# Performance work log

Hardware: AMD Instinct MI355X
Metric: run time of the kernel (lower is better)

Reference implementation:

```python
import jax, jax.numpy as jnp
import numpy as np

B, S, D, H, E, K, DH = 4, 2048, 1024, 8, 8, 2, 128
ROPE_BASE = 10000.0


def setup_inputs() -> dict:
    key = jax.random.key(0)
    ks = jax.random.split(key, 7)
    s = 1.0 / np.sqrt(D)
    x = jax.random.normal(ks[0], (B, S, D), dtype=jnp.float32)
    Wq = jax.random.normal(ks[1], (H * DH, D), dtype=jnp.float32) * s
    Wk = jax.random.normal(ks[2], (H * DH, D), dtype=jnp.float32) * s
    Wv = jax.random.normal(ks[3], (H * E, D, DH), dtype=jnp.float32) * s
    Wo = jax.random.normal(ks[4], (H * E, DH, D), dtype=jnp.float32) * (1.0 / np.sqrt(H * DH))
    sel_v = jax.random.normal(ks[5], (H * E, D), dtype=jnp.float32) * s
    sel_o = jax.random.normal(ks[6], (H * E, D), dtype=jnp.float32) * s
    positions = jnp.broadcast_to(jnp.arange(S, dtype=jnp.int32), (B, S))
    return {"x": x, "Wq": Wq, "Wk": Wk, "Wv": Wv, "Wo": Wo,
            "sel_v": sel_v, "sel_o": sel_o, "positions": positions}


def _rope(t, pos, inv_freq):
    # t: [b,h,s,d], pos: [b,s]
    freqs = pos.astype(t.dtype)[:, :, None] * inv_freq          # [b,s,d/2]
    emb = jnp.concatenate([freqs, freqs], axis=-1)[:, None]      # [b,1,s,d]
    sin, cos = jnp.sin(emb), jnp.cos(emb)
    x1, x2 = jnp.split(t, 2, axis=-1)
    rot = jnp.concatenate([-x2, x1], axis=-1)
    return t * cos + rot * sin


def reference(x, Wq, Wk, Wv, Wo, sel_v, sel_o, positions):
    # dense shared Q/K projections -> [b,h,s,dh]
    q = (x @ Wq.T).reshape(B, S, H, DH).transpose(0, 2, 1, 3)
    k = (x @ Wk.T).reshape(B, S, H, DH).transpose(0, 2, 1, 3)

    # V expert routing (sigmoid, non-competitive top-k per head)
    gv = jax.nn.sigmoid((x @ sel_v.T).reshape(B, S, H, E))       # [b,s,h,e]
    vw, vi = jax.lax.top_k(gv, K)                                # [b,s,h,k]
    vall = jnp.einsum('bsm,hemd->bshed', x, Wv.reshape(H, E, D, DH))
    vsel = jnp.take_along_axis(vall, vi[..., None], axis=3)      # [b,s,h,k,dh]
    v = (vw[..., None] * vsel).sum(axis=3).transpose(0, 2, 1, 3)  # [b,h,s,dh]

    # RoPE (rotate_fraction=1 -> full head dim)
    inv_freq = 1.0 / (ROPE_BASE ** (jnp.arange(0, DH, 2, dtype=jnp.float32) / DH))
    q = _rope(q, positions, inv_freq)
    k = _rope(k, positions, inv_freq)

    # masked SDPA (causal bool mask, scale 1/sqrt(dh))
    scores = jnp.einsum('bhqd,bhkd->bhqk', q, k) * (1.0 / np.sqrt(DH))
    causal = jnp.tril(jnp.ones((S, S), dtype=bool))
    scores = jnp.where(causal, scores, jnp.finfo(scores.dtype).min)
    attn = jax.nn.softmax(scores, axis=-1)
    ctx = jnp.einsum('bhqk,bhkd->bqhd', attn, v)                  # [b,s,h,dh]

    # O expert routing, combine via scattered gate weights
    go = jax.nn.sigmoid((x @ sel_o.T).reshape(B, S, H, E))
    ow, oi = jax.lax.top_k(go, K)
    g_full = (ow[..., None] * jax.nn.one_hot(oi, E, dtype=x.dtype)).sum(axis=3)  # [b,s,h,e]
    out = jnp.einsum('bshd,bshe,hedm->bsm', ctx, g_full, Wo.reshape(H, E, DH, D))
    return out
```

## Files before the change

### kernel.cpp

```cpp
#include <hip/hip_runtime.h>
#include <math.h>

typedef unsigned short u16;
typedef unsigned int u32;
typedef __attribute__((ext_vector_type(8))) short short8;
typedef __attribute__((ext_vector_type(4))) float f32x4;

constexpr int cB = 4, cS = 2048, cD = 1024, cH = 8, cE = 8, cK = 2, cDH = 128;
constexpr int cBS = cB * cS;
constexpr int cHE = cH * cE;

__device__ inline u16 f2bf(float f) {
    u32 u = __float_as_uint(f);
    u += 0x7fffu + ((u >> 16) & 1u);
    return (u16)(u >> 16);
}
__device__ inline float bf2f(u16 h) { return __uint_as_float(((u32)h) << 16); }

__device__ inline void gload_lds16(const u16* g, u16* l) {
    __builtin_amdgcn_global_load_lds(
        (const __attribute__((address_space(1))) void*)g,
        (__attribute__((address_space(3))) void*)l, 16, 0, 0);
}

#define SWZ_RD(row, ks, quad) ((((quad) + ((ks) >> 3)) ^ ((row) & 7)) << 3)

__global__ __launch_bounds__(256) void k_cast_split(
    const float* __restrict__ src, u16* __restrict__ hi, u16* __restrict__ lo)
{
    const size_t i = (size_t)blockIdx.x * 256 + threadIdx.x;
    float4 v = ((const float4*)src)[i];
    u16 hx = f2bf(v.x), hy = f2bf(v.y), hz = f2bf(v.z), hw = f2bf(v.w);
    u16 lx = f2bf(v.x - bf2f(hx)), ly = f2bf(v.y - bf2f(hy));
    u16 lz = f2bf(v.z - bf2f(hz)), lw = f2bf(v.w - bf2f(hw));
    uint2 oh; oh.x = (u32)hx | ((u32)hy << 16); oh.y = (u32)hz | ((u32)hw << 16);
    uint2 ol; ol.x = (u32)lx | ((u32)ly << 16); ol.y = (u32)lz | ((u32)lw << 16);
    ((uint2*)hi)[i] = oh;
    ((uint2*)lo)[i] = ol;
}

__global__ __launch_bounds__(256, 2) void k_gemm_logits3(
    const u16* __restrict__ xh, const u16* __restrict__ xlo,
    const u16* __restrict__ selh, const u16* __restrict__ sell,
    float* __restrict__ lgp)
{
    __shared__ u16 As[128 * 64];
    __shared__ u16 Bs[128 * 64];
    const int r0 = blockIdx.x * 128;
    const int term = blockIdx.y;
    const u16* A = (term == 1) ? xlo : xh;
    const u16* B = (term == 2) ? sell : selh;
    float* outp = lgp + (size_t)term * cBS * 128;
    const int t = threadIdx.x;
    const int w = t >> 6, lane = t & 63;
    const int wm = w >> 1, wn = w & 1;
    const int quad = lane >> 4, lm = lane & 15;
    const int lr = lane >> 3;
    const int lcs = (((lane & 7) ^ lr) * 8);

    f32x4 acc[4][4];
#pragma unroll
    for (int i = 0; i < 4; i++)
#pragma unroll
        for (int j = 0; j < 4; j++)
#pragma unroll
            for (int r = 0; r < 4; r++) acc[i][j][r] = 0.0f;

    for (int kc = 0; kc < cD; kc += 64) {
#pragma unroll
        for (int p = 0; p < 4; p++) {
            const int rA = p * 32 + w * 8;
            gload_lds16(A + (size_t)(r0 + rA + lr) * cD + kc + lcs, As + rA * 64);
            gload_lds16(B + (size_t)(rA + lr) * cD + kc + lcs, Bs + rA * 64);
        }
        __syncthreads();
#pragma unroll
        for (int ks = 0; ks < 64; ks += 32) {
            short8 av[4], bv[4];
#pragma unroll
            for (int i = 0; i < 4; i++) {
                const int row = wm * 64 + i * 16 + lm;
                av[i] = *(const short8*)(As + row * 64 + SWZ_RD(row, ks, quad));
            }
#pragma unroll
            for (int j = 0; j < 4; j++) {
                const int row = wn * 64 + j * 16 + lm;
                bv[j] = *(const short8*)(Bs + row * 64 + SWZ_RD(row, ks, quad));
            }
#pragma unroll
            for (int i = 0; i < 4; i++)
#pragma unroll
                for (int j = 0; j < 4; j++)
                    acc[i][j] = __builtin_amdgcn_mfma_f32_16x16x32_bf16(av[i], bv[j], acc[i][j], 0, 0, 0);
        }
        __syncthreads();
    }
#pragma unroll
    for (int i = 0; i < 4; i++)
#pragma unroll
        for (int r = 0; r < 4; r++) {
            const int row = r0 + wm * 64 + i * 16 + quad * 4 + r;
#pragma unroll
            for (int j = 0; j < 4; j++)
                outp[(size_t)row * 128 + wn * 64 + j * 16 + lm] = acc[i][j][r];
        }
}

__global__ __launch_bounds__(256) void k_top2_flag(
    const float* __restrict__ lgp, float* __restrict__ gv_d, float* __restrict__ go_d,
    int* __restrict__ flags, int* __restrict__ counter)
{
    const int idx = blockIdx.x * 256 + threadIdx.x;
    const int row = idx >> 4, r16 = idx & 15;
    const int which = r16 >> 3, h = r16 & 7;
    const float* l0 = lgp + (size_t)row * 128 + which * 64 + h * 8;
    const float* l1 = l0 + (size_t)cBS * 128;
    const float* l2 = l1 + (size_t)cBS * 128;
    float v[8];
#pragma unroll
    for (int e = 0; e < cE; e++) v[e] = l0[e] + l1[e] + l2[e];
    int i0 = 0; float b0 = v[0];
#pragma unroll
    for (int e = 1; e < cE; e++) { if (v[e] > b0) { b0 = v[e]; i0 = e; } }
    int i1 = -1; float b1 = -3.0e38f;
#pragma unroll
    for (int e = 0; e < cE; e++) { if (e != i0 && v[e] > b1) { b1 = v[e]; i1 = e; } }
    float b2 = -3.0e38f;
#pragma unroll
    for (int e = 0; e < cE; e++) { if (e != i0 && e != i1 && v[e] > b2) b2 = v[e]; }
    const float w0 = 1.0f / (1.0f + __expf(-b0));
    const float w1 = 1.0f / (1.0f + __expf(-b1));
    float* dst = (which ? go_d : gv_d) + (size_t)row * 64 + h * 8;
#pragma unroll
    for (int e = 0; e < cE; e++)
        dst[e] = (e == i0) ? w0 : ((e == i1) ? w1 : 0.0f);
    if (b1 - b2 < 1.0e-3f) {
        const int s = atomicAdd(counter, 1);
        flags[s] = (row << 4) | r16;
    }
}

__global__ __launch_bounds__(64) void k_repair(
    const float* __restrict__ x, const float* __restrict__ sel_v,
    const float* __restrict__ sel_o,
    const int* __restrict__ counter, const int* __restrict__ flags,
    float* __restrict__ gv_d, float* __restrict__ go_d)
{
    const int n = *counter;
    const int lane = threadIdx.x;
    for (int it = blockIdx.x; it < n; it += gridDim.x) {
        const int item = flags[it];
        const int row = item >> 4, which = (item >> 3) & 1, h = item & 7;
        const float* xr = x + (size_t)row * cD;
        const float* sb = (which ? sel_o : sel_v) + (size_t)(h * 8) * cD;
        float lg[8];
#pragma unroll
        for (int e = 0; e < cE; e++) {
            float a = 0.0f;
#pragma unroll
            for (int dg = 0; dg < 4; dg++) {
                const int d = dg * 256 + lane * 4;
                const float4 xv = *(const float4*)(xr + d);
                const float4 sv = *(const float4*)(sb + (size_t)e * cD + d);
                a += xv.x * sv.x + xv.y * sv.y + xv.z * sv.z + xv.w * sv.w;
            }
#pragma unroll
            for (int off = 1; off < 64; off <<= 1) a += __shfl_xor(a, off);
            lg[e] = a;
        }
        int i0 = 0; float b0 = lg[0];
#pragma unroll
        for (int e = 1; e < cE; e++) { if (lg[e] > b0) { b0 = lg[e]; i0 = e; } }
        int i1 = -1; float b1 = -3.0e38f;
#pragma unroll
        for (int e = 0; e < cE; e++) { if (e != i0 && lg[e] > b1) { b1 = lg[e]; i1 = e; } }
        if (lane == 0) {
            const float w0 = 1.0f / (1.0f + expf(-b0));
            const float w1 = 1.0f / (1.0f + expf(-b1));
            float* dst = (which ? go_d : gv_d) + (size_t)row * 64 + h * 8;
#pragma unroll
            for (int e = 0; e < cE; e++)
                dst[e] = (e == i0) ? w0 : ((e == i1) ? w1 : 0.0f);
        }
    }
}

__global__ __launch_bounds__(256) void k_cast_f2b(
    const float* __restrict__ src, u16* __restrict__ dst)
{
    const size_t i = (size_t)blockIdx.x * 256 + threadIdx.x;
    float4 v = ((const float4*)src)[i];
    u32 lo = (u32)f2bf(v.x) | ((u32)f2bf(v.y) << 16);
    u32 hi = (u32)f2bf(v.z) | ((u32)f2bf(v.w) << 16);
    uint2 o; o.x = lo; o.y = hi;
    ((uint2*)dst)[i] = o;
}

__global__ __launch_bounds__(256) void k_cast_wv(
    const float* __restrict__ Wv, u16* __restrict__ WvT)
{
    __shared__ float ld[64][132];
    const int d0 = blockIdx.x * 64, he = blockIdx.y;
    const int t = threadIdx.x;
    for (int p = 0; p < 8; p++) {
        const int slot = p * 256 + t, r = slot >> 5, c4 = slot & 31;
        float4 v = *(const float4*)(Wv + ((size_t)he * cD + d0 + r) * cDH + c4 * 4);
        ld[r][c4 * 4 + 0] = v.x; ld[r][c4 * 4 + 1] = v.y;
        ld[r][c4 * 4 + 2] = v.z; ld[r][c4 * 4 + 3] = v.w;
    }
    __syncthreads();
    for (int p = 0; p < 16; p++) {
        const int slot = p * 256 + t, dh = slot >> 5, c2 = slot & 31;
        u32 val = (u32)f2bf(ld[c2 * 2 + 0][dh]) | ((u32)f2bf(ld[c2 * 2 + 1][dh]) << 16);
        *(u32*)(WvT + (size_t)(he * cDH + dh) * cD + d0 + c2 * 2) = val;
    }
}

__global__ __launch_bounds__(256) void k_cast_wo(
    const float* __restrict__ Wo, u16* __restrict__ WoT)
{
    __shared__ float ld[128][68];
    const int m0 = blockIdx.x * 64, he = blockIdx.y;
    const int t = threadIdx.x;
    for (int p = 0; p < 8; p++) {
        const int slot = p * 256 + t, r = slot >> 4, c4 = slot & 15;
        float4 v = *(const float4*)(Wo + ((size_t)he * cDH + r) * cD + m0 + c4 * 4);
        ld[r][c4 * 4 + 0] = v.x; ld[r][c4 * 4 + 1] = v.y;
        ld[r][c4 * 4 + 2] = v.z; ld[r][c4 * 4 + 3] = v.w;
    }
    __syncthreads();
    for (int p = 0; p < 16; p++) {
        const int slot = p * 256 + t, mr = slot >> 6, c2 = slot & 63;
        u32 val = (u32)f2bf(ld[c2 * 2 + 0][mr]) | ((u32)f2bf(ld[c2 * 2 + 1][mr]) << 16);
        *(u32*)(WoT + (size_t)(m0 + mr) * 8192 + he * cDH + c2 * 2) = val;
    }
}

__global__ __launch_bounds__(256, 2) void k_gemm_v(
    const u16* __restrict__ xh, const u16* __restrict__ WvT,
    const float* __restrict__ gv_d, u16* __restrict__ v_b)
{
    __shared__ u16 As[128 * 72];
    __shared__ u16 Bs[128 * 72];
    __shared__ float Gs[128][9];
    const int rt = blockIdx.x, h = blockIdx.y;
    const int r0 = rt * 128;
    const int t = threadIdx.x;
    const int w = t >> 6, lane = t & 63;
    const int wm = w >> 1, wn = w & 1;
    const int quad = lane >> 4, lm = lane & 15;

    {
        const int row = t >> 1, half = t & 1;
        float4 g4 = *(const float4*)(gv_d + (size_t)(r0 + row) * 64 + h * 8 + half * 4);
        Gs[row][half * 4 + 0] = g4.x; Gs[row][half * 4 + 1] = g4.y;
        Gs[row][half * 4 + 2] = g4.z; Gs[row][half * 4 + 3] = g4.w;
    }

    f32x4 acc[4][4];
#pragma unroll
    for (int i = 0; i < 4; i++)
#pragma unroll
        for (int j = 0; j < 4; j++)
#pragma unroll
            for (int r = 0; r < 4; r++) acc[i][j][r] = 0.0f;

    for (int e = 0; e < cE; e++) {
        f32x4 acce[4][4];
#pragma unroll
        for (int i = 0; i < 4; i++)
#pragma unroll
            for (int j = 0; j < 4; j++)
#pragma unroll
                for (int r = 0; r < 4; r++) acce[i][j][r] = 0.0f;

        for (int kc = 0; kc < cD; kc += 64) {
#pragma unroll
            for (int p = 0; p < 4; p++) {
                const int slot = p * 256 + t, row = slot >> 3, seg = slot & 7;
                *(uint4*)(As + row * 72 + seg * 8) =
                    *(const uint4*)(xh + (size_t)(r0 + row) * cD + kc + seg * 8);
                *(uint4*)(Bs + row * 72 + seg * 8) =
                    *(const uint4*)(WvT + (size_t)((h * 8 + e) * cDH + row) * cD + kc + seg * 8);
            }
            __syncthreads();
#pragma unroll
            for (int ks = 0; ks < 64; ks += 32) {
                short8 av[4], bv[4];
#pragma unroll
                for (int i = 0; i < 4; i++)
                    av[i] = *(const short8*)(As + (wm * 64 + i * 16 + lm) * 72 + ks + quad * 8);
#pragma unroll
                for (int j = 0; j < 4; j++)
                    bv[j] = *(const short8*)(Bs + (wn * 64 + j * 16 + lm) * 72 + ks + quad * 8);
#pragma unroll
                for (int i = 0; i < 4; i++)
#pragma unroll
                    for (int j = 0; j < 4; j++)
                        acce[i][j] = __builtin_amdgcn_mfma_f32_16x16x32_bf16(av[i], bv[j], acce[i][j], 0, 0, 0);
            }
            __syncthreads();
        }
#pragma unroll
        for (int i = 0; i < 4; i++)
#pragma unroll
            for (int r = 0; r < 4; r++) {
                const float g = Gs[wm * 64 + i * 16 + quad * 4 + r][e];
#pragma unroll
                for (int j = 0; j < 4; j++) acc[i][j][r] += g * acce[i][j][r];
            }
    }
#pragma unroll
    for (int i = 0; i < 4; i++)
#pragma unroll
        for (int r = 0; r < 4; r++) {
            const int row = r0 + wm * 64 + i * 16 + quad * 4 + r;
            const int b = row >> 11, s = row & (cS - 1);
            u16* dst = v_b + ((size_t)(b * cH + h) * cS + s) * cDH;
#pragma unroll
            for (int j = 0; j < 4; j++)
                dst[wn * 64 + j * 16 + lm] = f2bf(acc[i][j][r]);
        }
}

__global__ __launch_bounds__(256, 2) void k_gemm_o(
    const u16* __restrict__ ctxh, const u16* __restrict__ WoT,
    const float* __restrict__ go_d, float* __restrict__ out)
{
    __shared__ u16 As[128 * 64];
    __shared__ u16 Bs[128 * 64];
    __shared__ float Gs[128][65];
    const int rt = blockIdx.x, nt = blockIdx.y;
    const int r0 = rt * 128;
    const int t = threadIdx.x;
    const int w = t >> 6, lane = t & 63;
    const int wm = w >> 1, wn = w & 1;
    const int quad = lane >> 4, lm = lane & 15;
    const int lr = lane >> 3;
    const int lcs = (((lane & 7) ^ lr) * 8);

#pragma unroll
    for (int p = 0; p < 8; p++) {
        const int slot = p * 256 + t, row = slot >> 4, seg = slot & 15;
        float4 g4 = *(const float4*)(go_d + (size_t)(r0 + row) * 64 + seg * 4);
        Gs[row][seg * 4 + 0] = g4.x; Gs[row][seg * 4 + 1] = g4.y;
        Gs[row][seg * 4 + 2] = g4.z; Gs[row][seg * 4 + 3] = g4.w;
    }

    f32x4 acc[4][4];
#pragma unroll
    for (int i = 0; i < 4; i++)
#pragma unroll
        for (int j = 0; j < 4; j++)
#pragma unroll
            for (int r = 0; r < 4; r++) acc[i][j][r] = 0.0f;

    for (int he = 0; he < cHE; he++) {
        f32x4 acce[4][4];
#pragma unroll
        for (int i = 0; i < 4; i++)
#pragma unroll
            for (int j = 0; j < 4; j++)
#pragma unroll
                for (int r = 0; r < 4; r++) acce[i][j][r] = 0.0f;

#pragma unroll
        for (int kc = 0; kc < 2; kc++) {
            const int ccol = (he >> 3) * 128 + kc * 64;
#pragma unroll
            for (int p = 0; p < 4; p++) {
                const int rA = p * 32 + w * 8;
                gload_lds16(ctxh + (size_t)(r0 + rA + lr) * cD + ccol + lcs, As + rA * 64);
                gload_lds16(WoT + (size_t)(nt * 128 + rA + lr) * 8192 + he * 128 + kc * 64 + lcs, Bs + rA * 64);
            }
            __syncthreads();
#pragma unroll
            for (int ks = 0; ks < 64; ks += 32) {
                short8 av[4], bv[4];
#pragma unroll
                for (int i = 0; i < 4; i++) {
                    const int row = wm * 64 + i * 16 + lm;
                    av[i] = *(const short8*)(As + row * 64 + SWZ_RD(row, ks, quad));
                }
#pragma unroll
                for (int j = 0; j < 4; j++) {
                    const int row = wn * 64 + j * 16 + lm;
                    bv[j] = *(const short8*)(Bs + row * 64 + SWZ_RD(row, ks, quad));
                }
#pragma unroll
                for (int i = 0; i < 4; i++)
#pragma unroll
                    for (int j = 0; j < 4; j++)
                        acce[i][j] = __builtin_amdgcn_mfma_f32_16x16x32_bf16(av[i], bv[j], acce[i][j], 0, 0, 0);
            }
            __syncthreads();
        }
#pragma unroll
        for (int i = 0; i < 4; i++)
#pragma unroll
            for (int r = 0; r < 4; r++) {
                const float g = Gs[wm * 64 + i * 16 + quad * 4 + r][he];
#pragma unroll
                for (int j = 0; j < 4; j++) acc[i][j][r] += g * acce[i][j][r];
            }
    }
#pragma unroll
    for (int i = 0; i < 4; i++)
#pragma unroll
        for (int r = 0; r < 4; r++) {
            const int row = r0 + wm * 64 + i * 16 + quad * 4 + r;
            float* dst = out + (size_t)row * cD + nt * 128;
#pragma unroll
            for (int j = 0; j < 4; j++)
                dst[wn * 64 + j * 16 + lm] = acc[i][j][r];
        }
}

__global__ __launch_bounds__(256, 2) void k_qkproj_mfma(
    const u16* __restrict__ xh, const u16* __restrict__ Wqb,
    const u16* __restrict__ Wkb, float* __restrict__ q_t, float* __restrict__ k_t)
{
    __shared__ u16 As[128 * 64];
    __shared__ u16 Bs[128 * 64];
    const int rt = blockIdx.x, nt = blockIdx.y;
    const bool isK = nt >= cH;
    const int h = isK ? nt - cH : nt;
    const u16* Wb = isK ? Wkb : Wqb;
    float* outp = isK ? k_t : q_t;
    const int r0 = rt * 128;
    const int t = threadIdx.x;
    const int w = t >> 6, lane = t & 63;
    const int wm = w >> 1, wn = w & 1;
    const int quad = lane >> 4, lm = lane & 15;
    const int lr = lane >> 3;
    const int lcs = (((lane & 7) ^ lr) * 8);

    f32x4 acc[4][4];
#pragma unroll
    for (int i = 0; i < 4; i++)
#pragma unroll
        for (int j = 0; j < 4; j++)
#pragma unroll
            for (int r = 0; r < 4; r++) acc[i][j][r] = 0.0f;

    for (int kc = 0; kc < cD; kc += 64) {
#pragma unroll
        for (int p = 0; p < 4; p++) {
            const int rA = p * 32 + w * 8;
            gload_lds16(xh + (size_t)(r0 + rA + lr) * cD + kc + lcs, As + rA * 64);
            gload_lds16(Wb + (size_t)(h * cDH + rA + lr) * cD + kc + lcs, Bs + rA * 64);
        }
        __syncthreads();
#pragma unroll
        for (int ks = 0; ks < 64; ks += 32) {
            short8 av[4], bv[4];
#pragma unroll
            for (int i = 0; i < 4; i++) {
                const int row = wm * 64 + i * 16 + lm;
                av[i] = *(const short8*)(As + row * 64 + SWZ_RD(row, ks, quad));
            }
#pragma unroll
            for (int j = 0; j < 4; j++) {
                const int row = wn * 64 + j * 16 + lm;
                bv[j] = *(const short8*)(Bs + row * 64 + SWZ_RD(row, ks, quad));
            }
#pragma unroll
            for (int i = 0; i < 4; i++)
#pragma unroll
                for (int j = 0; j < 4; j++)
                    acc[i][j] = __builtin_amdgcn_mfma_f32_16x16x32_bf16(av[i], bv[j], acc[i][j], 0, 0, 0);
        }
        __syncthreads();
    }
#pragma unroll
    for (int i = 0; i < 4; i++)
#pragma unroll
        for (int r = 0; r < 4; r++) {
            const int row = r0 + wm * 64 + i * 16 + quad * 4 + r;
            const int b = row >> 11, s = row & (cS - 1);
            float* dst = outp + ((size_t)(b * cH + h) * cS + s) * cDH;
#pragma unroll
            for (int j = 0; j < 4; j++)
                dst[wn * 64 + j * 16 + lm] = acc[i][j][r];
        }
}

__global__ __launch_bounds__(256) void k_rope_cast(
    const float* __restrict__ q_t, const float* __restrict__ k_t,
    const int* __restrict__ positions,
    u16* __restrict__ q_b, u16* __restrict__ k_b)
{
    const int total = cB * cH * cS * (cDH / 2);
    const int idx = blockIdx.x * 256 + threadIdx.x;
    const int which = (idx >= total) ? 1 : 0;
    const int id = which ? idx - total : idx;
    const int i = id & 63;
    const int bhs = id >> 6;
    const int s = bhs & (cS - 1);
    const int b = (bhs >> 11) >> 3;
    const float* src = (which ? k_t : q_t) + (size_t)bhs * cDH;
    u16* dst = (which ? k_b : q_b) + (size_t)bhs * cDH;
    const int pos = positions[b * cS + s];
    const float freq = exp2f((float)i * -0.20762050593745932f);
    const float ang = (float)pos * freq;
    float sn, c;
    __sincosf(ang, &sn, &c);
    const float t1 = src[i], t2 = src[i + 64];
    dst[i] = f2bf(t1 * c - t2 * sn);
    dst[i + 64] = f2bf(t2 * c + t1 * sn);
}

__global__ __launch_bounds__(256, 2) void k_attn_mfma(
    const u16* __restrict__ qb, const u16* __restrict__ kb,
    const u16* __restrict__ vb, u16* __restrict__ ctxh)
{
    __shared__ u16 Ks[64][136];
    __shared__ u16 VsT[128][72];
    __shared__ u16 Ps[4][32][72];

    const int combined = blockIdx.z * 8 + blockIdx.y;
    const int qtv = (combined < 16) ? (15 - (int)blockIdx.x) : (int)blockIdx.x;
    const int h = blockIdx.y, b = blockIdx.z;
    const int q0 = qtv * 128;
    const int t = threadIdx.x;
    const int w = t >> 6, lane = t & 63;
    const int quad = lane >> 4, lm = lane & 15;
    const size_t bh = (size_t)(b * cH + h) * cS;
    const u16* kbase = kb + bh * cDH;
    const u16* vbase = vb + bh * cDH;

    short8 aq[2][4];
#pragma unroll
    for (int mi = 0; mi < 2; mi++) {
        const u16* qrow = qb + (bh + q0 + w * 32 + mi * 16 + lm) * cDH;
#pragma unroll
        for (int ks = 0; ks < 4; ks++)
            aq[mi][ks] = *(const short8*)(qrow + ks * 32 + quad * 8);
    }

    f32x4 o_acc[2][8];
#pragma unroll
    for (int mi = 0; mi < 2; mi++)
#pragma unroll
        for (int j = 0; j < 8; j++)
#pragma unroll
            for (int r = 0; r < 4; r++) o_acc[mi][j][r] = 0.0f;
    float m_r[2][4], l_r[2][4];
#pragma unroll
    for (int mi = 0; mi < 2; mi++)
#pragma unroll
        for (int r = 0; r < 4; r++) { m_r[mi][r] = -1.0e30f; l_r[mi][r] = 0.0f; }
    const float scale = 0.08838834764831845f;
    const int nkt = 2 * qtv + 2;

    for (int kt = 0; kt < nkt; kt++) {
        const int k0 = kt * 64;
#pragma unroll
        for (int p = 0; p < 4; p++) {
            const int slot = p * 256 + t, row = slot >> 4, seg = slot & 15;
            *(uint4*)&Ks[row][seg * 8] =
                *(const uint4*)(kbase + (size_t)(k0 + row) * cDH + seg * 8);
        }
        {
            const int rq = t & 15, seg = t >> 4;
            uint4 r0v = *(const uint4*)(vbase + (size_t)(k0 + rq * 4 + 0) * cDH + seg * 8);
            uint4 r1v = *(const uint4*)(vbase + (size_t)(k0 + rq * 4 + 1) * cDH + seg * 8);
            uint4 r2v = *(const uint4*)(vbase + (size_t)(k0 + rq * 4 + 2) * cDH + seg * 8);
            uint4 r3v = *(const uint4*)(vbase + (size_t)(k0 + rq * 4 + 3) * cDH + seg * 8);
            const u16* p0 = (const u16*)&r0v; const u16* p1 = (const u16*)&r1v;
            const u16* p2 = (const u16*)&r2v; const u16* p3 = (const u16*)&r3v;
#pragma unroll
            for (int jj = 0; jj < 8; jj++) {
                ushort4 val;
                val.x = p0[jj]; val.y = p1[jj]; val.z = p2[jj]; val.w = p3[jj];
                *(ushort4*)&VsT[seg * 8 + jj][rq * 4] = val;
            }
        }
        __syncthreads();

        f32x4 s[2][4];
#pragma unroll
        for (int mi = 0; mi < 2; mi++)
#pragma unroll
            for (int j = 0; j < 4; j++)
#pragma unroll
                for (int r = 0; r < 4; r++) s[mi][j][r] = 0.0f;
#pragma unroll
        for (int ks = 0; ks < 4; ks++) {
#pragma unroll
            for (int j = 0; j < 4; j++) {
                short8 bv = *(const short8*)&Ks[j * 16 + lm][ks * 32 + quad * 8];
                s[0][j] = __builtin_amdgcn_mfma_f32_16x16x32_bf16(aq[0][ks], bv, s[0][j], 0, 0, 0);
                s[1][j] = __builtin_amdgcn_mfma_f32_16x16x32_bf16(aq[1][ks], bv, s[1][j], 0, 0, 0);
            }
        }
        if (kt >= nkt - 2) {
#pragma unroll
            for (int mi = 0; mi < 2; mi++)
#pragma unroll
                for (int j = 0; j < 4; j++) {
                    const int colg = k0 + j * 16 + lm;
#pragma unroll
                    for (int r = 0; r < 4; r++) {
                        const int rowg = q0 + w * 32 + mi * 16 + quad * 4 + r;
                        s[mi][j][r] = (colg <= rowg) ? s[mi][j][r] * scale : -1.0e30f;
                    }
                }
        } else {
#pragma unroll
            for (int mi = 0; mi < 2; mi++)
#pragma unroll
                for (int j = 0; j < 4; j++)
#pragma unroll
                    for (int r = 0; r < 4; r++) s[mi][j][r] *= scale;
        }
#pragma unroll
        for (int mi = 0; mi < 2; mi++) {
            float mt[4];
#pragma unroll
            for (int r = 0; r < 4; r++)
                mt[r] = fmaxf(fmaxf(s[mi][0][r], s[mi][1][r]), fmaxf(s[mi][2][r], s[mi][3][r]));
#pragma unroll
            for (int off = 1; off < 16; off <<= 1)
#pragma unroll
                for (int r = 0; r < 4; r++) mt[r] = fmaxf(mt[r], __shfl_xor(mt[r], off));
            float alpha[4], rs[4];
#pragma unroll
            for (int r = 0; r < 4; r++) {
                const float mn = fmaxf(m_r[mi][r], mt[r]);
                alpha[r] = __expf(m_r[mi][r] - mn);
                m_r[mi][r] = mn;
                rs[r] = 0.0f;
            }
#pragma unroll
            for (int j = 0; j < 4; j++)
#pragma unroll
                for (int r = 0; r < 4; r++) {
                    const float p = __expf(s[mi][j][r] - m_r[mi][r]);
                    s[mi][j][r] = p;
                    rs[r] += p;
                }
#pragma unroll
            for (int off = 1; off < 16; off <<= 1)
#pragma unroll
                for (int r = 0; r < 4; r++) rs[r] += __shfl_xor(rs[r], off);
#pragma unroll
            for (int r = 0; r < 4; r++) l_r[mi][r] = l_r[mi][r] * alpha[r] + rs[r];
#pragma unroll
            for (int j = 0; j < 8; j++)
#pragma unroll
                for (int r = 0; r < 4; r++) o_acc[mi][j][r] *= alpha[r];
#pragma unroll
            for (int j = 0; j < 4; j++)
#pragma unroll
                for (int r = 0; r < 4; r++)
                    Ps[w][mi * 16 + quad * 4 + r][j * 16 + lm] = f2bf(s[mi][j][r]);
        }
#pragma unroll
        for (int ks2 = 0; ks2 < 2; ks2++) {
            short8 ap0 = *(const short8*)&Ps[w][lm][ks2 * 32 + quad * 8];
            short8 ap1 = *(const short8*)&Ps[w][16 + lm][ks2 * 32 + quad * 8];
#pragma unroll
            for (int j2 = 0; j2 < 8; j2++) {
                short8 bv = *(const short8*)&VsT[j2 * 16 + lm][ks2 * 32 + quad * 8];
                o_acc[0][j2] = __builtin_amdgcn_mfma_f32_16x16x32_bf16(ap0, bv, o_acc[0][j2], 0, 0, 0);
                o_acc[1][j2] = __builtin_amdgcn_mfma_f32_16x16x32_bf16(ap1, bv, o_acc[1][j2], 0, 0, 0);
            }
        }
        __syncthreads();
    }
#pragma unroll
    for (int mi = 0; mi < 2; mi++)
#pragma unroll
        for (int r = 0; r < 4; r++) {
            const float inv = 1.0f / l_r[mi][r];
            const int sg = q0 + w * 32 + mi * 16 + quad * 4 + r;
            u16* dst = ctxh + (((size_t)b * cS + sg) * cH + h) * cDH;
#pragma unroll
            for (int j2 = 0; j2 < 8; j2++)
                dst[j2 * 16 + lm] = f2bf(o_acc[mi][j2][r] * inv);
        }
}

extern "C" void kernel_launch(void* const* d_in, const int* in_sizes, int n_in,
                              void* d_out, int out_size, void* d_ws, size_t ws_size,
                              hipStream_t stream)
{
    const float* x = (const float*)d_in[0];
    const float* Wq = (const float*)d_in[1];
    const float* Wk = (const float*)d_in[2];
    const float* Wv = (const float*)d_in[3];
    const float* Wo = (const float*)d_in[4];
    const float* sel_v = (const float*)d_in[5];
    const float* sel_o = (const float*)d_in[6];
    const int* positions = (const int*)d_in[7];
    float* out = (float*)d_out;

    char* ws = (char*)d_ws;
    size_t off = 0;
    auto alloc = [&](size_t bytes) -> void* {
        void* p = ws + off;
        off += (bytes + 255) & ~(size_t)255;
        return p;
    };
    const size_t big = (size_t)cB * cH * cS * cDH * sizeof(float);
    const size_t half = big / 2;
    char* R1 = (char*)alloc(big);
    char* R2 = (char*)alloc(big);
    char* R3 = (char*)alloc(big);
    char* R4 = (char*)alloc(big);
    float* gv_d = (float*)alloc((size_t)cBS * 64 * sizeof(float));
    float* go_d = (float*)alloc((size_t)cBS * 64 * sizeof(float));
    u16* selh = (u16*)alloc((size_t)128 * cD * sizeof(u16));
    u16* sell = (u16*)alloc((size_t)128 * cD * sizeof(u16));
    int* flags = (int*)alloc((size_t)cBS * 16 * sizeof(int));
    int* counter = (int*)alloc(256);

    u16* WvT = (u16*)R1;
    float* lgp = (float*)(R1 + half);
    float* q_t = (float*)R1;
    u16* xlo = (u16*)R2;
    float* k_t = (float*)R2;
    u16* WoT = (u16*)R2;
    u16* v_b = (u16*)R3;
    u16* Wqb = (u16*)(R3 + half);
    u16* Wkb = (u16*)(R3 + half + ((size_t)cD * cD * 2));
    u16* ctxh = (u16*)(R3 + half);
    u16* xh = (u16*)R4;
    u16* q_b = (u16*)R4;
    u16* k_b = (u16*)(R4 + half);

    hipMemsetAsync(counter, 0, sizeof(int), stream);

    k_cast_split<<<8192, 256, 0, stream>>>(x, xh, xlo);
    k_cast_split<<<64, 256, 0, stream>>>(sel_v, selh, sell);
    k_cast_split<<<64, 256, 0, stream>>>(sel_o, selh + (size_t)cHE * cD,
                                         sell + (size_t)cHE * cD);
    k_gemm_logits3<<<dim3(64, 3), 256, 0, stream>>>(xh, xlo, selh, sell, lgp);
    k_top2_flag<<<512, 256, 0, stream>>>(lgp, gv_d, go_d, flags, counter);
    k_repair<<<256, 64, 0, stream>>>(x, sel_v, sel_o, counter, flags, gv_d, go_d);

    k_cast_wv<<<dim3(16, 64), 256, 0, stream>>>(Wv, WvT);
    k_gemm_v<<<dim3(64, 8), 256, 0, stream>>>(xh, WvT, gv_d, v_b);

    k_cast_f2b<<<1024, 256, 0, stream>>>(Wq, Wqb);
    k_cast_f2b<<<1024, 256, 0, stream>>>(Wk, Wkb);
    k_qkproj_mfma<<<dim3(64, 16), 256, 0, stream>>>(xh, Wqb, Wkb, q_t, k_t);
    k_rope_cast<<<(2 * cB * cH * cS * (cDH / 2)) / 256, 256, 0, stream>>>(
        q_t, k_t, positions, q_b, k_b);
    k_attn_mfma<<<dim3(16, 8, 4), 256, 0, stream>>>(q_b, k_b, v_b, ctxh);

    k_cast_wo<<<dim3(16, 64), 256, 0, stream>>>(Wo, WoT);
    k_gemm_o<<<dim3(64, 8), 256, 0, stream>>>(ctxh, WoT, go_d, out);
}
```

Before: 686.6 us.

## Widen V-GEMM K-chunk and reuse ctx tile across experts in O-GEMM

The V expert GEMM now stages 128-wide K chunks instead of 64, which halves the number of barrier-separated load and compute rounds. The O expert GEMM is restructured as a head loop over an expert loop. The ctx A-tile (the full 128-wide head slice) and that head's gate values are loaded once per head and reused across all 8 experts, so only the Wo tile is reloaded per expert. This cuts redundant global-to-LDS traffic and halves barriers in the O GEMM, at the cost of more LDS per block, which may lower occupancy.

```diff
diff --git a/kernel.cpp b/kernel.cpp
--- a/kernel.cpp
+++ b/kernel.cpp
@@ -240,8 +240,8 @@
     const u16* __restrict__ xh, const u16* __restrict__ WvT,
     const float* __restrict__ gv_d, u16* __restrict__ v_b)
 {
-    __shared__ u16 As[128 * 72];
-    __shared__ u16 Bs[128 * 72];
+    __shared__ u16 As[128 * 136];
+    __shared__ u16 Bs[128 * 136];
     __shared__ float Gs[128][9];
     const int rt = blockIdx.x, h = blockIdx.y;
     const int r0 = rt * 128;
@@ -274,25 +274,25 @@
 #pragma unroll
                 for (int r = 0; r < 4; r++) acce[i][j][r] = 0.0f;
 
-        for (int kc = 0; kc < cD; kc += 64) {
-#pragma unroll
-            for (int p = 0; p < 4; p++) {
-                const int slot = p * 256 + t, row = slot >> 3, seg = slot & 7;
-                *(uint4*)(As + row * 72 + seg * 8) =
+        for (int kc = 0; kc < cD; kc += 128) {
+#pragma unroll
+            for (int p = 0; p < 8; p++) {
+                const int slot = p * 256 + t, row = slot >> 4, seg = slot & 15;
+                *(uint4*)(As + row * 136 + seg * 8) =
                     *(const uint4*)(xh + (size_t)(r0 + row) * cD + kc + seg * 8);
-                *(uint4*)(Bs + row * 72 + seg * 8) =
+                *(uint4*)(Bs + row * 136 + seg * 8) =
                     *(const uint4*)(WvT + (size_t)((h * 8 + e) * cDH + row) * cD + kc + seg * 8);
             }
             __syncthreads();
 #pragma unroll
-            for (int ks = 0; ks < 64; ks += 32) {
+            for (int ks = 0; ks < 128; ks += 32) {
                 short8 av[4], bv[4];
 #pragma unroll
                 for (int i = 0; i < 4; i++)
-                    av[i] = *(const short8*)(As + (wm * 64 + i * 16 + lm) * 72 + ks + quad * 8);
+                    av[i] = *(const short8*)(As + (wm * 64 + i * 16 + lm) * 136 + ks + quad * 8);
 #pragma unroll
                 for (int j = 0; j < 4; j++)
-                    bv[j] = *(const short8*)(Bs + (wn * 64 + j * 16 + lm) * 72 + ks + quad * 8);
+                    bv[j] = *(const short8*)(Bs + (wn * 64 + j * 16 + lm) * 136 + ks + quad * 8);
 #pragma unroll
                 for (int i = 0; i < 4; i++)
 #pragma unroll
@@ -327,9 +327,9 @@
     const u16* __restrict__ ctxh, const u16* __restrict__ WoT,
     const float* __restrict__ go_d, float* __restrict__ out)
 {
-    __shared__ u16 As[128 * 64];
-    __shared__ u16 Bs[128 * 64];
-    __shared__ float Gs[128][65];
+    __shared__ u16 As[2][128 * 64];
+    __shared__ u16 Bs[2][128 * 64];
+    __shared__ float Gs[128][9];
     const int rt = blockIdx.x, nt = blockIdx.y;
     const int r0 = rt * 128;
     const int t = threadIdx.x;
@@ -339,14 +339,6 @@
     const int lr = lane >> 3;
     const int lcs = (((lane & 7) ^ lr) * 8);
 
-#pragma unroll
-    for (int p = 0; p < 8; p++) {
-        const int slot = p * 256 + t, row = slot >> 4, seg = slot & 15;
-        float4 g4 = *(const float4*)(go_d + (size_t)(r0 + row) * 64 + seg * 4);
-        Gs[row][seg * 4 + 0] = g4.x; Gs[row][seg * 4 + 1] = g4.y;
-        Gs[row][seg * 4 + 2] = g4.z; Gs[row][seg * 4 + 3] = g4.w;
-    }
-
     f32x4 acc[4][4];
 #pragma unroll
     for (int i = 0; i < 4; i++)
@@ -355,54 +347,71 @@
 #pragma unroll
             for (int r = 0; r < 4; r++) acc[i][j][r] = 0.0f;
 
-    for (int he = 0; he < cHE; he++) {
-        f32x4 acce[4][4];
-#pragma unroll
-        for (int i = 0; i < 4; i++)
-#pragma unroll
-            for (int j = 0; j < 4; j++)
-#pragma unroll
-                for (int r = 0; r < 4; r++) acce[i][j][r] = 0.0f;
-
-#pragma unroll
-        for (int kc = 0; kc < 2; kc++) {
-            const int ccol = (he >> 3) * 128 + kc * 64;
-#pragma unroll
-            for (int p = 0; p < 4; p++) {
-                const int rA = p * 32 + w * 8;
-                gload_lds16(ctxh + (size_t)(r0 + rA + lr) * cD + ccol + lcs, As + rA * 64);
-                gload_lds16(WoT + (size_t)(nt * 128 + rA + lr) * 8192 + he * 128 + kc * 64 + lcs, Bs + rA * 64);
-            }
+    for (int h = 0; h < cH; h++) {
+        for (int e = 0; e < cE; e++) {
+            const int he = h * 8 + e;
+            if (e == 0) {
+#pragma unroll
+                for (int kc = 0; kc < 2; kc++)
+#pragma unroll
+                    for (int p = 0; p < 4; p++) {
+                        const int rA = p * 32 + w * 8;
+                        gload_lds16(ctxh + (size_t)(r0 + rA + lr) * cD + h * 128 + kc * 64 + lcs,
+                                    As[kc] + rA * 64);
+                    }
+                const int row = t >> 1, half = t & 1;
+                float4 g4 = *(const float4*)(go_d + (size_t)(r0 + row) * 64 + h * 8 + half * 4);
+                Gs[row][half * 4 + 0] = g4.x; Gs[row][half * 4 + 1] = g4.y;
+                Gs[row][half * 4 + 2] = g4.z; Gs[row][half * 4 + 3] = g4.w;
+            }
+#pragma unroll
+            for (int kc = 0; kc < 2; kc++)
+#pragma unroll
+                for (int p = 0; p < 4; p++) {
+                    const int rA = p * 32 + w * 8;
+                    gload_lds16(WoT + (size_t)(nt * 128 + rA + lr) * 8192 + he * 128 + kc * 64 + lcs,
+                                Bs[kc] + rA * 64);
+                }
             __syncthreads();
-#pragma unroll
-            for (int ks = 0; ks < 64; ks += 32) {
-                short8 av[4], bv[4];
-#pragma unroll
-                for (int i = 0; i < 4; i++) {
-                    const int row = wm * 64 + i * 16 + lm;
-                    av[i] = *(const short8*)(As + row * 64 + SWZ_RD(row, ks, quad));
+
+            f32x4 acce[4][4];
+#pragma unroll
+            for (int i = 0; i < 4; i++)
+#pragma unroll
+                for (int j = 0; j < 4; j++)
+#pragma unroll
+                    for (int r = 0; r < 4; r++) acce[i][j][r] = 0.0f;
+#pragma unroll
+            for (int kc = 0; kc < 2; kc++)
+#pragma unroll
+                for (int ks = 0; ks < 64; ks += 32) {
+                    short8 av[4], bv[4];
+#pragma unroll
+                    for (int i = 0; i < 4; i++) {
+                        const int row = wm * 64 + i * 16 + lm;
+                        av[i] = *(const short8*)(As[kc] + row * 64 + SWZ_RD(row, ks, quad));
+                    }
+#pragma unroll
+                    for (int j = 0; j < 4; j++) {
+                        const int row = wn * 64 + j * 16 + lm;
+                        bv[j] = *(const short8*)(Bs[kc] + row * 64 + SWZ_RD(row, ks, quad));
+                    }
+#pragma unroll
+                    for (int i = 0; i < 4; i++)
+#pragma unroll
+                        for (int j = 0; j < 4; j++)
+                            acce[i][j] = __builtin_amdgcn_mfma_f32_16x16x32_bf16(av[i], bv[j], acce[i][j], 0, 0, 0);
                 }
 #pragma unroll
-                for (int j = 0; j < 4; j++) {
-                    const int row = wn * 64 + j * 16 + lm;
-                    bv[j] = *(const short8*)(Bs + row * 64 + SWZ_RD(row, ks, quad));
+            for (int i = 0; i < 4; i++)
+#pragma unroll
+                for (int r = 0; r < 4; r++) {
+                    const float g = Gs[wm * 64 + i * 16 + quad * 4 + r][e];
+#pragma unroll
+                    for (int j = 0; j < 4; j++) acc[i][j][r] += g * acce[i][j][r];
                 }
-#pragma unroll
-                for (int i = 0; i < 4; i++)
-#pragma unroll
-                    for (int j = 0; j < 4; j++)
-                        acce[i][j] = __builtin_amdgcn_mfma_f32_16x16x32_bf16(av[i], bv[j], acce[i][j], 0, 0, 0);
-            }
             __syncthreads();
         }
-#pragma unroll
-        for (int i = 0; i < 4; i++)
-#pragma unroll
-            for (int r = 0; r < 4; r++) {
-                const float g = Gs[wm * 64 + i * 16 + quad * 4 + r][he];
-#pragma unroll
-                for (int j = 0; j < 4; j++) acc[i][j][r] += g * acce[i][j][r];
-            }
     }
 #pragma unroll
     for (int i = 0; i < 4; i++)
```

New measurement: 801.7 us. +16.8%, slower.
